# Performance work log

Measured on AMD Instinct MI355X. Metric: run time of the kernel, lower is better.

The kernel has to match this reference:

```python
import jax, jax.numpy as jnp
import numpy as np

N_NODES, IN_DIM, HID, LAT, N_EDGES = 50000, 3000, 512, 30, 800000
NEG_SLOPE = 0.2


def setup_inputs() -> dict:
    key = jax.random.key(0)
    ks = jax.random.split(key, 6)
    x = jax.random.normal(ks[0], (N_NODES, IN_DIM), dtype=jnp.float32)
    edge_index = jax.random.randint(ks[1], (2, N_EDGES), 0, N_NODES, dtype=jnp.int64)
    # xavier-normal-ish scales
    W1 = jax.random.normal(ks[2], (IN_DIM, HID), dtype=jnp.float32) * 0.02
    W2 = jax.random.normal(ks[3], (HID, LAT), dtype=jnp.float32) * 0.06
    att_src = jax.random.normal(ks[4], (HID,), dtype=jnp.float32) * 0.1
    att_dst = jax.random.normal(ks[5], (HID,), dtype=jnp.float32) * 0.1
    return {"x": x, "edge_index": edge_index, "W1": W1, "W2": W2,
            "att_src": att_src, "att_dst": att_dst}


def _segment_softmax(e, seg, num_segments):
    # numerically stable softmax over variable-degree dst neighborhoods
    m = jax.ops.segment_max(e, seg, num_segments=num_segments)
    m = jnp.where(jnp.isfinite(m), m, 0.0)  # empty segments -> 0, harmless
    p = jnp.exp(e - m[seg])
    s = jax.ops.segment_sum(p, seg, num_segments=num_segments)
    return p / (s[seg] + 1e-16)


def reference(x, edge_index, W1, W2, att_src, att_dst):
    N = x.shape[0]
    src, dst = edge_index[0], edge_index[1]  # messages flow src(j) -> dst(i)

    # ---- conv1: full GAT layer (heads=1, no self-loops, no bias) ----
    h1 = x @ W1                                   # [N, 512]
    a_src = h1 @ att_src                          # [N]
    a_dst = h1 @ att_dst                          # [N]
    e = jax.nn.leaky_relu(a_src[src] + a_dst[dst], NEG_SLOPE)  # [E]
    alpha = _segment_softmax(e, dst, N)           # [E] (also tied attn for conv3)
    agg1 = jax.ops.segment_sum(h1[src] * alpha[:, None], dst, num_segments=N)
    x1 = jax.nn.elu(agg1)                         # [N, 512]

    # ---- conv2: attention=False -> plain linear projection ----
    x2 = x1 @ W2                                  # [N, 30] (latent embedding)

    # ---- conv3: tied weights (W2^T) + tied attention from conv1 ----
    h3 = x2 @ W2.T                                # [N, 512]
    agg3 = jax.ops.segment_sum(h3[src] * alpha[:, None], dst, num_segments=N)
    x3 = jax.nn.elu(agg3)

    # ---- conv4: attention=False, tied weights (W1^T) ----
    x4 = x3 @ W1.T                                # [N, in_channels]
    return (x2, x4)
```

## Files before the change

### kernel.cpp

```cpp
#include <hip/hip_runtime.h>

#define N_NODES 50000
#define IN_DIM  3000
#define HID     512
#define LAT     30
#define N_EDGES 800000
#define M_PAD   50048
#define K1_PAD  3008
#define N4_PAD  3072

typedef __bf16 bf16;
typedef unsigned int uint;
typedef __attribute__((ext_vector_type(4))) float f32x4;
typedef __attribute__((ext_vector_type(8))) bf16 bf16x8;

__device__ __forceinline__ float bf2f(bf16 b){ return (float)b; }

__device__ __forceinline__ void gl16(const void* g, void* l){
  __builtin_amdgcn_global_load_lds(
      (const __attribute__((address_space(1))) void*)g,
      (__attribute__((address_space(3))) void*)l, 16, 0, 0);
}

__device__ __forceinline__ int xcd_swz(int orig, int nwg){
  int q = nwg >> 3, r = nwg & 7;
  int xcd = orig & 7, lid = orig >> 3;
  return (xcd < r ? xcd*(q+1) : r*(q+1) + (xcd-r)*q) + lid;
}

__device__ __forceinline__ bf16x8 cvt8v(f32x4 a, f32x4 b){
  bf16x8 r;
  r[0]=(bf16)a[0]; r[1]=(bf16)a[1]; r[2]=(bf16)a[2]; r[3]=(bf16)a[3];
  r[4]=(bf16)b[0]; r[5]=(bf16)b[1]; r[6]=(bf16)b[2]; r[7]=(bf16)b[3];
  return r;
}

__global__ void k_w1t(const float* __restrict__ W1, bf16* __restrict__ W1T){
  int k = blockIdx.x*256 + threadIdx.x;
  int n = blockIdx.y;
  if (k >= K1_PAD) return;
  float v = (k < IN_DIM) ? W1[(long)k*HID + n] : 0.f;
  W1T[(long)n*K1_PAD + k] = (bf16)v;
}
__global__ void k_w1p(const float* __restrict__ W1, bf16* __restrict__ W1P){
  int k = blockIdx.x*256 + threadIdx.x;
  int n = blockIdx.y;
  if (k >= HID) return;
  float v = (n < IN_DIM) ? W1[(long)n*HID + k] : 0.f;
  W1P[(long)n*HID + k] = (bf16)v;
}
__global__ void k_w2t(const float* __restrict__ W2, bf16* __restrict__ W2T){
  int k = blockIdx.x*256 + threadIdx.x;
  int n = blockIdx.y;
  if (k >= HID) return;
  float v = (n < LAT) ? W2[(long)k*LAT + n] : 0.f;
  W2T[(long)n*HID + k] = (bf16)v;
}
__global__ void k_w2p(const float* __restrict__ W2, bf16* __restrict__ W2P){
  int t = blockIdx.x*256 + threadIdx.x;
  if (t >= HID*32) return;
  int n = t >> 5, k = t & 31;
  W2P[t] = (bf16)((k < LAT) ? W2[(long)n*LAT + k] : 0.f);
}

__global__ __launch_bounds__(256) void gemm_xw1(
    const float* __restrict__ X, const bf16* __restrict__ Bw, bf16* __restrict__ C)
{
  __shared__ float Af[128*32];
  __shared__ bf16  Bl[128*32];
  const int NBX = HID/128;
  const int tid  = threadIdx.x;
  const int lane = tid & 63;
  const int w    = tid >> 6;
  const int wm   = (w >> 1) * 64, wn = (w & 1) * 64;
  const int wgid = xcd_swz(blockIdx.x, gridDim.x);
  const int col0 = (wgid % NBX) * 128, row0 = (wgid / NBX) * 128;

  f32x4 acc[4][4];
  #pragma unroll
  for (int mi=0;mi<4;mi++)
    #pragma unroll
    for (int ni=0;ni<4;ni++)
      acc[mi][ni] = (f32x4){0.f,0.f,0.f,0.f};

  const int ar  = tid >> 3;
  const int apc = tid & 7;
  const int ac4 = (apc ^ (ar & 7)) * 4;
  int aoff[4];
  #pragma unroll
  for (int i=0;i<4;i++)
    aoff[i] = min(row0 + i*32 + ar, N_NODES-1) * IN_DIM;

  const int sr = tid >> 2;
  const int sc = (tid & 3) * 16;
  const char* gB = (const char*)(Bw + (long)(col0 + sr) * K1_PAD) + sc;
  const long bstep = (long)64 * K1_PAD * 2;
  float* lA = Af + tid*4;
  char*  lB = (char*)Bl + sr*64 + sc;

  for (int ks = 0; ks < 94; ks++){
    int kcl = min(ks*32 + ac4, IN_DIM-4);
    #pragma unroll
    for (int i=0;i<4;i++)
      gl16(X + aoff[i] + kcl, lA + i*1024);
    gl16(gB + (long)ks*64,         lB);
    gl16(gB + (long)ks*64 + bstep, lB + 64*64);
    __syncthreads();

    const int g2 = (lane >> 4) * 2;
    bf16x8 af[4], bfr[4];
    #pragma unroll
    for (int mi=0;mi<4;mi++){
      int row = wm + mi*16 + (lane & 15);
      int rx  = row & 7;
      f32x4 f0 = *(const f32x4*)&Af[row*32 + ((g2    ) ^ rx)*4];
      f32x4 f1 = *(const f32x4*)&Af[row*32 + ((g2 + 1) ^ rx)*4];
      af[mi] = cvt8v(f0, f1);
    }
    #pragma unroll
    for (int ni=0;ni<4;ni++)
      bfr[ni] = *(const bf16x8*)&Bl[(wn + ni*16 + (lane & 15))*32 + (lane>>4)*8];
    #pragma unroll
    for (int mi=0;mi<4;mi++)
      #pragma unroll
      for (int ni=0;ni<4;ni++)
        acc[mi][ni] = __builtin_amdgcn_mfma_f32_16x16x32_bf16(af[mi], bfr[ni], acc[mi][ni], 0, 0, 0);
    __syncthreads();
  }

  const int crb  = (lane >> 4) * 4;
  const int ccol = lane & 15;
  #pragma unroll
  for (int mi=0;mi<4;mi++){
    #pragma unroll
    for (int v=0;v<4;v++){
      int r = row0 + wm + mi*16 + crb + v;
      if (r >= N_NODES) continue;
      #pragma unroll
      for (int ni=0;ni<4;ni++){
        int cc = col0 + wn + ni*16 + ccol;
        C[(long)r*HID + cc] = (bf16)acc[mi][ni][v];
      }
    }
  }
}

template<bool C_F32, bool ELU>
__global__ __launch_bounds__(256) void gemm_glds(
    const bf16* __restrict__ A, const bf16* __restrict__ B, void* __restrict__ Cp,
    int lda, int ldb, int Ksteps, int Mvalid, int Nvalid, int ldc, int NBX)
{
  __shared__ bf16 Alds[128*32];
  __shared__ bf16 Blds[128*32];
  const int tid  = threadIdx.x;
  const int lane = tid & 63;
  const int w    = tid >> 6;
  const int wm   = (w >> 1) * 64, wn = (w & 1) * 64;
  const int wgid = xcd_swz(blockIdx.x, gridDim.x);
  const int col0 = (wgid % NBX) * 128, row0 = (wgid / NBX) * 128;

  f32x4 acc[4][4];
  #pragma unroll
  for (int mi=0;mi<4;mi++)
    #pragma unroll
    for (int ni=0;ni<4;ni++)
      acc[mi][ni] = (f32x4){0.f,0.f,0.f,0.f};

  const int sr = tid >> 2;
  const int sc = (tid & 3) * 16;

  const char* ga = (const char*)(A + (long)(row0 + sr) * lda) + sc;
  const char* gb = (const char*)(B + (long)(col0 + sr) * ldb) + sc;
  char* la = (char*)Alds + sr*64 + sc;
  char* lb = (char*)Blds + sr*64 + sc;
  const long astep = (long)64 * lda * 2;
  const long bstep = (long)64 * ldb * 2;

  for (int ks = 0; ks < Ksteps; ks++){
    const long ko = (long)ks * 64;
    gl16(ga + ko,         la);
    gl16(ga + ko + astep, la + 64*64);
    gl16(gb + ko,         lb);
    gl16(gb + ko + bstep, lb + 64*64);
    __syncthreads();

    bf16x8 af[4], bfr[4];
    #pragma unroll
    for (int mi=0;mi<4;mi++)
      af[mi] = *(const bf16x8*)&Alds[(wm + mi*16 + (lane & 15))*32 + (lane>>4)*8];
    #pragma unroll
    for (int ni=0;ni<4;ni++)
      bfr[ni] = *(const bf16x8*)&Blds[(wn + ni*16 + (lane & 15))*32 + (lane>>4)*8];
    #pragma unroll
    for (int mi=0;mi<4;mi++)
      #pragma unroll
      for (int ni=0;ni<4;ni++)
        acc[mi][ni] = __builtin_amdgcn_mfma_f32_16x16x32_bf16(af[mi], bfr[ni], acc[mi][ni], 0, 0, 0);
    __syncthreads();
  }

  const int crb  = (lane >> 4) * 4;
  const int ccol = lane & 15;
  #pragma unroll
  for (int mi=0;mi<4;mi++){
    #pragma unroll
    for (int v=0;v<4;v++){
      int r = row0 + wm + mi*16 + crb + v;
      if (r >= Mvalid) continue;
      #pragma unroll
      for (int ni=0;ni<4;ni++){
        int c = col0 + wn + ni*16 + ccol;
        if (c >= Nvalid) continue;
        float val = acc[mi][ni][v];
        if (ELU) val = (val > 0.f) ? val : expm1f(val);
        if (C_F32) ((float*)Cp)[(long)r*ldc + c] = val;
        else       ((bf16*)Cp)[(long)r*ldc + c] = (bf16)val;
      }
    }
  }
}

__global__ void k_attdots(const bf16* __restrict__ h1, const float* __restrict__ att_s,
                          const float* __restrict__ att_d, float* __restrict__ a_src,
                          float* __restrict__ a_dst){
  int gid = blockIdx.x * blockDim.x + threadIdx.x;
  int row = gid >> 6, lane = gid & 63;
  if (row >= N_NODES) return;
  bf16x8 hv = *(const bf16x8*)(h1 + (long)row*HID + lane*8);
  float s1 = 0.f, s2 = 0.f;
  #pragma unroll
  for (int j=0;j<8;j++){
    float h = bf2f(hv[j]);
    s1 = fmaf(h, att_s[lane*8+j], s1);
    s2 = fmaf(h, att_d[lane*8+j], s2);
  }
  #pragma unroll
  for (int o=32;o>0;o>>=1){ s1 += __shfl_down(s1,o); s2 += __shfl_down(s2,o); }
  if (lane == 0){ a_src[row] = s1; a_dst[row] = s2; }
}

__global__ void k_deg(const int* __restrict__ ei, int* __restrict__ deg){
  int e = blockIdx.x*256 + threadIdx.x;
  if (e >= N_EDGES) return;
  atomicAdd(&deg[ei[N_EDGES + e]], 1);
}

__global__ void k_scan(const int* __restrict__ deg, int* __restrict__ off, int* __restrict__ cur){
  const int n = M_PAD, T = 1024;
  int t = threadIdx.x;
  const int per = (n + T - 1) / T;
  int s0 = t*per, s1 = min(n, s0+per);
  int sum = 0;
  for (int i=s0;i<s1;i++) sum += deg[i];
  __shared__ int sd[1024];
  sd[t] = sum; __syncthreads();
  for (int o=1;o<T;o<<=1){
    int x = (t>=o) ? sd[t-o] : 0;
    __syncthreads();
    sd[t] += x;
    __syncthreads();
  }
  int run = sd[t] - sum;
  for (int i=s0;i<s1;i++){
    off[i] = run; cur[i] = run;
    run += deg[i];
  }
  if (s0 < n && s1 == n) off[n] = run;
}

__global__ void k_fill(const int* __restrict__ ei, int* __restrict__ cur,
                       int* __restrict__ csr_src, const float* __restrict__ a_s,
                       const float* __restrict__ a_d, float* __restrict__ p_e){
  int e = blockIdx.x*256 + threadIdx.x;
  if (e >= N_EDGES) return;
  int s = ei[e];
  int d = ei[N_EDGES + e];
  int pos = atomicAdd(&cur[d], 1);
  csr_src[pos] = s;
  float v = a_s[s] + a_d[d];
  v = (v > 0.f) ? v : 0.2f*v;
  p_e[pos] = __expf(v);
}

__global__ __launch_bounds__(512) void k_agg1(
    const int* __restrict__ off, const int* __restrict__ csr_src,
    const float* __restrict__ p_edge,
    const bf16* __restrict__ h1, bf16* __restrict__ x1,
    float* __restrict__ s_node)
{
  const int i = blockIdx.x;
  const int t = threadIdx.x;
  const int start = off[i];
  const int deg = off[i+1] - start;
  __shared__ float p_sh[512];
  __shared__ int   s_sh[512];

  float acc = 0.f, ssum = 0.f;
  for (int base=0; base<deg; base+=512){
    int cnt = min(512, deg-base);
    if (t < cnt){
      p_sh[t] = p_edge[start+base+t];
      s_sh[t] = csr_src[start+base+t];
    }
    __syncthreads();
    for (int k=0;k<cnt;k++){
      float pk = p_sh[k];
      ssum += pk;
      acc = fmaf(pk, bf2f(h1[(long)s_sh[k]*HID + t]), acc);
    }
    __syncthreads();
  }
  float val = acc / (ssum + 1e-16f);
  val = (val > 0.f) ? val : expm1f(val);
  x1[(long)i*HID + t] = (bf16)val;
  if (t == 0) s_node[i] = ssum;
}

__global__ void k_agg3(const int* __restrict__ off, const int* __restrict__ csr_src,
                       const float* __restrict__ p_edge, const float* __restrict__ s_node,
                       const float* __restrict__ x2, bf16* __restrict__ aggb)
{
  int i = blockIdx.x*8 + (threadIdx.x >> 5);
  int lane = threadIdx.x & 31;
  if (i >= M_PAD) return;
  float acc = 0.f;
  if (i < N_NODES){
    int s0 = off[i], d = off[i+1] - s0;
    for (int k=0;k<d;k++){
      int s = csr_src[s0+k];
      float pk = p_edge[s0+k];
      if (lane < LAT) acc = fmaf(pk, x2[(long)s*LAT + lane], acc);
    }
    acc *= 1.f/(s_node[i] + 1e-16f);
  }
  aggb[(long)i*32 + lane] = (bf16)((lane < LAT) ? acc : 0.f);
}

extern "C" void kernel_launch(void* const* d_in, const int* in_sizes, int n_in,
                              void* d_out, int out_size, void* d_ws, size_t ws_size,
                              hipStream_t stream)
{
  const float* x     = (const float*)d_in[0];
  const int*   ei    = (const int*)d_in[1];
  const float* W1    = (const float*)d_in[2];
  const float* W2    = (const float*)d_in[3];
  const float* att_s = (const float*)d_in[4];
  const float* att_d = (const float*)d_in[5];

  float* out_x2 = (float*)d_out;
  float* out_x4 = (float*)d_out + (long)N_NODES*LAT;

  bf16* h1 = (bf16*)out_x4;
  bf16* x1 = h1 + (long)M_PAD*HID;

  char* w = (char*)d_ws;
  bf16* W1T = (bf16*)w;  w += (long)HID*K1_PAD*2;
  bf16* W1P = (bf16*)w;  w += (long)N4_PAD*HID*2;
  bf16* W2T = (bf16*)w;  w += (long)128*HID*2;
  bf16* W2P = (bf16*)w;  w += (long)HID*32*2;
  bf16* x3  = (bf16*)w;  w += (long)M_PAD*HID*2;
  bf16* aggb= (bf16*)w;  w += (long)M_PAD*32*2;
  int* deg  = (int*)w;   w += (long)M_PAD*4;
  int* offs = (int*)w;   w += (long)(M_PAD+64)*4;
  int* cur  = (int*)w;   w += (long)M_PAD*4;
  int* csr  = (int*)w;   w += (long)N_EDGES*4;
  float* p_e = (float*)w; w += (long)N_EDGES*4;
  float* s_n = (float*)w; w += (long)M_PAD*4;
  float* a_s = (float*)w; w += (long)M_PAD*4;
  float* a_d = (float*)w; w += (long)M_PAD*4;

  k_w1t<<<dim3((K1_PAD+255)/256, HID), 256, 0, stream>>>(W1, W1T);
  k_w1p<<<dim3((HID+255)/256, N4_PAD), 256, 0, stream>>>(W1, W1P);
  k_w2t<<<dim3(2, 128), 256, 0, stream>>>(W2, W2T);
  k_w2p<<<(HID*32+255)/256, 256, 0, stream>>>(W2, W2P);

  hipMemsetAsync(deg, 0, (size_t)M_PAD*4, stream);
  k_deg<<<(N_EDGES+255)/256, 256, 0, stream>>>(ei, deg);
  k_scan<<<1, 1024, 0, stream>>>(deg, offs, cur);

  gemm_xw1<<<(M_PAD/128)*(HID/128), 256, 0, stream>>>(x, W1T, h1);

  k_attdots<<<(N_NODES*64)/256, 256, 0, stream>>>(h1, att_s, att_d, a_s, a_d);

  k_fill<<<(N_EDGES+255)/256, 256, 0, stream>>>(ei, cur, csr, a_s, a_d, p_e);

  k_agg1<<<N_NODES, 512, 0, stream>>>(offs, csr, p_e, h1, x1, s_n);

  gemm_glds<true,false><<<1*(M_PAD/128), 256, 0, stream>>>(
      x1, W2T, out_x2, HID, HID, HID/32, N_NODES, LAT, LAT, 1);

  k_agg3<<<(M_PAD+7)/8, 256, 0, stream>>>(offs, csr, p_e, s_n, out_x2, aggb);
  gemm_glds<false,true><<<(HID/128)*(M_PAD/128), 256, 0, stream>>>(
      aggb, W2P, x3, 32, 32, 1, M_PAD, HID, HID, HID/128);

  gemm_glds<true,false><<<(N4_PAD/128)*(M_PAD/128), 256, 0, stream>>>(
      x3, W1P, out_x4, HID, HID, HID/32, N_NODES, IN_DIM, IN_DIM, N4_PAD/128);
}
```

Before: 1.217 ms.

## Double-buffer LDS tiles in GEMM kernels to overlap global loads with MFMA

Both GEMM kernels (the fp32-input X@W1 GEMM and the generic bf16 GEMM) now keep two LDS buffers for the A and B tiles. The next K-step's global-to-LDS loads are issued before the MFMAs on the current tile, with one vmcnt wait and barrier per iteration instead of two syncthreads. This is meant to hide global memory latency behind compute, at the cost of twice the LDS per block, which may reduce occupancy.

```diff
diff --git a/kernel.cpp b/kernel.cpp
--- a/kernel.cpp
+++ b/kernel.cpp
@@ -66,8 +66,8 @@
 __global__ __launch_bounds__(256) void gemm_xw1(
     const float* __restrict__ X, const bf16* __restrict__ Bw, bf16* __restrict__ C)
 {
-  __shared__ float Af[128*32];
-  __shared__ bf16  Bl[128*32];
+  __shared__ float Af[2][128*32];
+  __shared__ bf16  Bl[2][128*32];
   const int NBX = HID/128;
   const int tid  = threadIdx.x;
   const int lane = tid & 63;
@@ -95,38 +95,51 @@
   const int sc = (tid & 3) * 16;
   const char* gB = (const char*)(Bw + (long)(col0 + sr) * K1_PAD) + sc;
   const long bstep = (long)64 * K1_PAD * 2;
-  float* lA = Af + tid*4;
-  char*  lB = (char*)Bl + sr*64 + sc;
+
+#define STAGE1(buf, ks) do{                                             \
+    int kcl_ = min((ks)*32 + ac4, IN_DIM-4);                            \
+    char* lA_ = (char*)&Af[buf][0] + tid*16;                            \
+    _Pragma("unroll")                                                   \
+    for (int i_=0;i_<4;i_++)                                            \
+      gl16(X + aoff[i_] + kcl_, lA_ + i_*4096);                         \
+    char* lB_ = (char*)&Bl[buf][0] + sr*64 + sc;                        \
+    gl16(gB + (long)(ks)*64,         lB_);                              \
+    gl16(gB + (long)(ks)*64 + bstep, lB_ + 64*64);                      \
+  }while(0)
+
+  STAGE1(0, 0);
+  asm volatile("s_waitcnt vmcnt(0)" ::: "memory");
+  __builtin_amdgcn_s_barrier();
 
   for (int ks = 0; ks < 94; ks++){
-    int kcl = min(ks*32 + ac4, IN_DIM-4);
-    #pragma unroll
-    for (int i=0;i<4;i++)
-      gl16(X + aoff[i] + kcl, lA + i*1024);
-    gl16(gB + (long)ks*64,         lB);
-    gl16(gB + (long)ks*64 + bstep, lB + 64*64);
-    __syncthreads();
-
+    const int cur = ks & 1;
+    if (ks + 1 < 94) STAGE1(cur^1, ks+1);
+
+    const float* Ac = &Af[cur][0];
+    const bf16*  Bc = &Bl[cur][0];
     const int g2 = (lane >> 4) * 2;
     bf16x8 af[4], bfr[4];
     #pragma unroll
     for (int mi=0;mi<4;mi++){
       int row = wm + mi*16 + (lane & 15);
       int rx  = row & 7;
-      f32x4 f0 = *(const f32x4*)&Af[row*32 + ((g2    ) ^ rx)*4];
-      f32x4 f1 = *(const f32x4*)&Af[row*32 + ((g2 + 1) ^ rx)*4];
+      f32x4 f0 = *(const f32x4*)&Ac[row*32 + ((g2    ) ^ rx)*4];
+      f32x4 f1 = *(const f32x4*)&Ac[row*32 + ((g2 + 1) ^ rx)*4];
       af[mi] = cvt8v(f0, f1);
     }
     #pragma unroll
     for (int ni=0;ni<4;ni++)
-      bfr[ni] = *(const bf16x8*)&Bl[(wn + ni*16 + (lane & 15))*32 + (lane>>4)*8];
+      bfr[ni] = *(const bf16x8*)&Bc[(wn + ni*16 + (lane & 15))*32 + (lane>>4)*8];
     #pragma unroll
     for (int mi=0;mi<4;mi++)
       #pragma unroll
       for (int ni=0;ni<4;ni++)
         acc[mi][ni] = __builtin_amdgcn_mfma_f32_16x16x32_bf16(af[mi], bfr[ni], acc[mi][ni], 0, 0, 0);
-    __syncthreads();
-  }
+
+    asm volatile("s_waitcnt vmcnt(0)" ::: "memory");
+    __builtin_amdgcn_s_barrier();
+  }
+#undef STAGE1
 
   const int crb  = (lane >> 4) * 4;
   const int ccol = lane & 15;
@@ -150,8 +163,8 @@
     const bf16* __restrict__ A, const bf16* __restrict__ B, void* __restrict__ Cp,
     int lda, int ldb, int Ksteps, int Mvalid, int Nvalid, int ldc, int NBX)
 {
-  __shared__ bf16 Alds[128*32];
-  __shared__ bf16 Blds[128*32];
+  __shared__ bf16 Alds[2][128*32];
+  __shared__ bf16 Blds[2][128*32];
   const int tid  = threadIdx.x;
   const int lane = tid & 63;
   const int w    = tid >> 6;
@@ -171,33 +184,46 @@
 
   const char* ga = (const char*)(A + (long)(row0 + sr) * lda) + sc;
   const char* gb = (const char*)(B + (long)(col0 + sr) * ldb) + sc;
-  char* la = (char*)Alds + sr*64 + sc;
-  char* lb = (char*)Blds + sr*64 + sc;
   const long astep = (long)64 * lda * 2;
   const long bstep = (long)64 * ldb * 2;
 
+#define STAGE2(buf, ks) do{                                             \
+    const long ko_ = (long)(ks) * 64;                                   \
+    char* la_ = (char*)&Alds[buf][0] + sr*64 + sc;                      \
+    char* lb_ = (char*)&Blds[buf][0] + sr*64 + sc;                      \
+    gl16(ga + ko_,         la_);                                        \
+    gl16(ga + ko_ + astep, la_ + 64*64);                                \
+    gl16(gb + ko_,         lb_);                                        \
+    gl16(gb + ko_ + bstep, lb_ + 64*64);                                \
+  }while(0)
+
+  STAGE2(0, 0);
+  asm volatile("s_waitcnt vmcnt(0)" ::: "memory");
+  __builtin_amdgcn_s_barrier();
+
   for (int ks = 0; ks < Ksteps; ks++){
-    const long ko = (long)ks * 64;
-    gl16(ga + ko,         la);
-    gl16(ga + ko + astep, la + 64*64);
-    gl16(gb + ko,         lb);
-    gl16(gb + ko + bstep, lb + 64*64);
-    __syncthreads();
-
+    const int cur = ks & 1;
+    if (ks + 1 < Ksteps) STAGE2(cur^1, ks+1);
+
+    const bf16* Ac = &Alds[cur][0];
+    const bf16* Bc = &Blds[cur][0];
     bf16x8 af[4], bfr[4];
     #pragma unroll
     for (int mi=0;mi<4;mi++)
-      af[mi] = *(const bf16x8*)&Alds[(wm + mi*16 + (lane & 15))*32 + (lane>>4)*8];
+      af[mi] = *(const bf16x8*)&Ac[(wm + mi*16 + (lane & 15))*32 + (lane>>4)*8];
     #pragma unroll
     for (int ni=0;ni<4;ni++)
-      bfr[ni] = *(const bf16x8*)&Blds[(wn + ni*16 + (lane & 15))*32 + (lane>>4)*8];
+      bfr[ni] = *(const bf16x8*)&Bc[(wn + ni*16 + (lane & 15))*32 + (lane>>4)*8];
     #pragma unroll
     for (int mi=0;mi<4;mi++)
       #pragma unroll
       for (int ni=0;ni<4;ni++)
         acc[mi][ni] = __builtin_amdgcn_mfma_f32_16x16x32_bf16(af[mi], bfr[ni], acc[mi][ni], 0, 0, 0);
-    __syncthreads();
-  }
+
+    asm volatile("s_waitcnt vmcnt(0)" ::: "memory");
+    __builtin_amdgcn_s_barrier();
+  }
+#undef STAGE2
 
   const int crb  = (lane >> 4) * 4;
   const int ccol = lane & 15;
```

Result: slower. 1.281 ms (+5.2%).
